# Optimization experiments

Measured on AMD Instinct MI355X. Metric: run time of the kernel, lower is better.

## Reference

```python
import jax, jax.numpy as jnp
import numpy as np

B, N, C = 2, 2048, 1024
H = 16
D = C // H  # head_dim = 64
HID = 4 * C
EPS = 1e-5


def _layernorm(x, g, b):
    mu = jnp.mean(x, axis=-1, keepdims=True)
    var = jnp.var(x, axis=-1, keepdims=True)
    return (x - mu) * jax.lax.rsqrt(var + EPS) * g + b


def _rope(x):
    # x: (B, H, N, D); interleaved-pair rotation, sin/cos computed in fp32
    half = D // 2
    inv_freq = 1.0 / (10000.0 ** (jnp.arange(half, dtype=jnp.float32) / half))
    pos = jnp.arange(N, dtype=jnp.float32)
    freqs = pos[:, None] * inv_freq[None, :]            # (N, half)
    sin = jnp.sin(freqs).astype(x.dtype)
    cos = jnp.cos(freqs).astype(x.dtype)
    xr = x.reshape(*x.shape[:-1], half, 2)
    x1, x2 = xr[..., 0], xr[..., 1]
    r1 = x1 * cos - x2 * sin
    r2 = x1 * sin + x2 * cos
    return jnp.stack((r1, r2), axis=-1).reshape(x.shape)


def setup_inputs() -> dict:
    key = jax.random.key(0)
    ks = jax.random.split(key, 8)
    s = lambda d: 1.0 / np.sqrt(d)
    return {
        "x": jax.random.normal(ks[0], (B, N, C), jnp.float32),
        "ln1_g": jnp.ones((C,), jnp.float32),
        "ln1_b": jnp.zeros((C,), jnp.float32),
        "W_qkv": jax.random.normal(ks[1], (C, 3 * C), jnp.float32) * s(C),
        "b_qkv": jnp.zeros((3 * C,), jnp.float32),
        "W_proj": jax.random.normal(ks[2], (C, C), jnp.float32) * s(C),
        "b_proj": jnp.zeros((C,), jnp.float32),
        "ln2_g": jnp.ones((C,), jnp.float32),
        "ln2_b": jnp.zeros((C,), jnp.float32),
        "W_fc1": jax.random.normal(ks[3], (C, HID), jnp.float32) * s(C),
        "b_fc1": jnp.zeros((HID,), jnp.float32),
        "W_fc2": jax.random.normal(ks[4], (HID, C), jnp.float32) * s(HID),
        "b_fc2": jnp.zeros((C,), jnp.float32),
    }


def reference(x, ln1_g, ln1_b, W_qkv, b_qkv, W_proj, b_proj,
              ln2_g, ln2_b, W_fc1, b_fc1, W_fc2, b_fc2):
    # --- attention branch ---
    h = _layernorm(x, ln1_g, ln1_b)
    qkv = h @ W_qkv + b_qkv                              # (B, N, 3C)
    qkv = qkv.reshape(B, N, 3, H, D).transpose(2, 0, 3, 1, 4)
    q, k, v = qkv[0], qkv[1], qkv[2]                     # each (B, H, N, D)
    q = _rope(q)
    k = _rope(k)
    scale = D ** -0.5
    attn = jnp.einsum('bhnd,bhmd->bhnm', q, k) * scale
    attn = jax.nn.softmax(attn, axis=-1)
    o = jnp.einsum('bhnm,bhmd->bhnd', attn, v)           # (B, H, N, D)
    o = o.transpose(0, 2, 1, 3).reshape(B, N, C)
    x = x + (o @ W_proj + b_proj)
    # --- MLP branch ---
    h = _layernorm(x, ln2_g, ln2_b)
    h = jax.nn.gelu(h @ W_fc1 + b_fc1, approximate=False)
    x = x + (h @ W_fc2 + b_fc2)
    return x
```

## Files before the change

kernel.cpp:

```cpp
#include <hip/hip_runtime.h>
#include <cstdint>
#include <cstddef>

typedef unsigned short u16;
typedef unsigned int   u32;
typedef __attribute__((ext_vector_type(8))) short v8s;
typedef __attribute__((ext_vector_type(4))) float v4f;

#define B_   2
#define N_   2048
#define C_   1024
#define H_   16
#define D_   64
#define HID_ 4096
#define M_   4096

static __device__ __forceinline__ float b2f(u32 u) {
    union { u32 i; float f; } x; x.i = u << 16; return x.f;
}
static __device__ __forceinline__ u16 f2b(float f) {
    union { float f; u32 i; } x; x.f = f;
    u32 r = (x.i + 0x7fffu + ((x.i >> 16) & 1u)) >> 16;
    return (u16)r;
}
static __device__ __forceinline__ u32 scale2(u32 raw, float s) {
    float lo = b2f(raw & 0xffffu) * s, hi = b2f(raw >> 16) * s;
    return (u32)f2b(lo) | ((u32)f2b(hi) << 16);
}

static __device__ __forceinline__ void gload_lds16(const u16* g, u16* l) {
    __builtin_amdgcn_global_load_lds(
        (const __attribute__((address_space(1))) void*)g,
        (__attribute__((address_space(3))) void*)l,
        16, 0, 0);
}

static __device__ __forceinline__ int2 xcd_swz(int gx, int gy) {
    const int nwg = gx * gy;
    int id = blockIdx.y * gx + blockIdx.x;
    id = (id & 7) * (nwg >> 3) + (id >> 3);
    return make_int2(id % gx, id / gx);
}

__global__ __launch_bounds__(256) void transpose_all(const float* __restrict__ Wqkv,
                                                     const float* __restrict__ Wproj,
                                                     const float* __restrict__ Wfc1,
                                                     const float* __restrict__ Wfc2,
                                                     u16* __restrict__ Oqkv,
                                                     u16* __restrict__ Oproj,
                                                     u16* __restrict__ Ofc1,
                                                     u16* __restrict__ Ofc2) {
    __shared__ float tile[32][33];
    int id = blockIdx.x;
    const float* in; u16* out; int K, N, nx;
    if (id < 3072)      { in = Wqkv;  out = Oqkv;  K = 1024; N = 3072; nx = 96;  }
    else if (id < 4096) { in = Wproj; out = Oproj; K = 1024; N = 1024; nx = 32;  id -= 3072; }
    else if (id < 8192) { in = Wfc1;  out = Ofc1;  K = 1024; N = 4096; nx = 128; id -= 4096; }
    else                { in = Wfc2;  out = Ofc2;  K = 4096; N = 1024; nx = 32;  id -= 8192; }
    const int n0 = (id % nx) * 32, k0 = (id / nx) * 32;
    const int c = threadIdx.x & 31, r8 = threadIdx.x >> 5;
#pragma unroll
    for (int i = 0; i < 4; ++i)
        tile[r8 + i * 8][c] = in[(size_t)(k0 + r8 + i * 8) * N + n0 + c];
    __syncthreads();
#pragma unroll
    for (int i = 0; i < 4; ++i)
        out[(size_t)(n0 + r8 + i * 8) * K + k0 + c] = f2b(tile[c][r8 + i * 8]);
}

__global__ __launch_bounds__(256) void ln_kernel(const float* __restrict__ in,
                                                 const float* __restrict__ g,
                                                 const float* __restrict__ b,
                                                 u16* __restrict__ out) {
    __shared__ float ps[4], psq[4];
    __shared__ float stats[2];
    const int row = blockIdx.x;
    const int t = threadIdx.x;
    float4 v = ((const float4*)in)[(size_t)row * 256 + t];
    float s  = v.x + v.y + v.z + v.w;
    float sq = v.x * v.x + v.y * v.y + v.z * v.z + v.w * v.w;
#pragma unroll
    for (int off = 32; off > 0; off >>= 1) { s += __shfl_down(s, off); sq += __shfl_down(sq, off); }
    if ((t & 63) == 0) { ps[t >> 6] = s; psq[t >> 6] = sq; }
    __syncthreads();
    if (t == 0) {
        float S = ps[0] + ps[1] + ps[2] + ps[3];
        float Q = psq[0] + psq[1] + psq[2] + psq[3];
        float mu  = S * (1.f / 1024.f);
        float var = Q * (1.f / 1024.f) - mu * mu;
        stats[0] = mu; stats[1] = rsqrtf(var + 1e-5f);
    }
    __syncthreads();
    const float mu = stats[0], istd = stats[1];
    float4 gg = ((const float4*)g)[t];
    float4 bb = ((const float4*)b)[t];
    ushort4 o;
    o.x = f2b((v.x - mu) * istd * gg.x + bb.x);
    o.y = f2b((v.y - mu) * istd * gg.y + bb.y);
    o.z = f2b((v.z - mu) * istd * gg.z + bb.z);
    o.w = f2b((v.w - mu) * istd * gg.w + bb.w);
    *(ushort4*)&out[(size_t)row * 1024 + t * 4] = o;
}

__global__ __launch_bounds__(256) void rope_table(float2* __restrict__ tab) {
    const int i = blockIdx.x * 256 + threadIdx.x;
    const int d = i & 31, n = i >> 5;
    float inv = powf(10000.f, -(float)d * (1.f / 32.f));
    float fr = (float)n * inv;
    tab[i] = make_float2(cosf(fr), sinf(fr));
}

template <int EPI, int BM>
__global__ __launch_bounds__(256) void gemm_bt(const u16* __restrict__ A,
                                               const u16* __restrict__ Bt,
                                               const float* __restrict__ bias,
                                               void* __restrict__ outp,
                                               const float* __restrict__ resid,
                                               const float2* __restrict__ tab,
                                               int Ndim, int Kdim) {
    constexpr int NACC = (BM == 128) ? 4 : 2;
    constexpr int AISS = BM / 64;
    __shared__ u16 As[3][BM * 32];
    __shared__ u16 Bs[3][128 * 32];
    const int t = threadIdx.x;
    const int lane = t & 63;
    const int w = t >> 6;
    const int wr = (BM == 128) ? (w >> 1) : 0;
    const int wc = (BM == 128) ? (w & 1) : w;
    const int2 lb = xcd_swz(gridDim.x, gridDim.y);
    const int m0 = lb.y * BM, n0 = lb.x * 128;
    const int hi = lane >> 4, lo = lane & 15;

    auto STAGE = [&](int buf, int kt) {
#pragma unroll
        for (int j = 0; j < AISS; ++j) {
            const int c = (w * AISS + j) * 64 + lane;
            gload_lds16(&A[(size_t)(m0 + (c >> 2)) * Kdim + kt + (c & 3) * 8],
                        &As[buf][(w * AISS + j) * 512]);
        }
#pragma unroll
        for (int j = 0; j < 2; ++j) {
            const int c = (w * 2 + j) * 64 + lane;
            gload_lds16(&Bt[(size_t)(n0 + (c >> 2)) * Kdim + kt + (c & 3) * 8],
                        &Bs[buf][(w * 2 + j) * 512]);
        }
    };

    const v4f vzero = {0.f, 0.f, 0.f, 0.f};
    v4f acc[4][NACC];
#pragma unroll
    for (int i = 0; i < 4; ++i)
#pragma unroll
        for (int j = 0; j < NACC; ++j) acc[i][j] = vzero;

    const int nt = Kdim / 32;
    STAGE(0, 0);
    STAGE(1, 32);
    for (int kt = 0; kt < nt; ++kt) {
        if constexpr (BM == 128) asm volatile("s_waitcnt vmcnt(4)" ::: "memory");
        else                     asm volatile("s_waitcnt vmcnt(3)" ::: "memory");
        __builtin_amdgcn_s_barrier();
        if (kt + 2 < nt) STAGE((kt + 2) % 3, (kt + 2) * 32);
        const int cur = kt % 3;
        v8s av[4], bv[NACC];
#pragma unroll
        for (int mi = 0; mi < 4; ++mi)
            av[mi] = *(const v8s*)&As[cur][(wr * 64 + mi * 16 + lo) * 32 + hi * 8];
#pragma unroll
        for (int ni = 0; ni < NACC; ++ni)
            bv[ni] = *(const v8s*)&Bs[cur][(wc * (NACC * 16) + ni * 16 + lo) * 32 + hi * 8];
#pragma unroll
        for (int mi = 0; mi < 4; ++mi)
#pragma unroll
            for (int ni = 0; ni < NACC; ++ni)
                acc[mi][ni] = __builtin_amdgcn_mfma_f32_16x16x32_bf16(av[mi], bv[ni], acc[mi][ni], 0, 0, 0);
    }

#pragma unroll
    for (int mi = 0; mi < 4; ++mi)
#pragma unroll
        for (int ni = 0; ni < NACC; ++ni) {
            const int col = n0 + wc * (NACC * 16) + ni * 16 + lo;
            const float bsv = bias[col];
#pragma unroll
            for (int r = 0; r < 4; ++r) {
                const int row = m0 + wr * 64 + mi * 16 + hi * 4 + r;
                float vacc = acc[mi][ni][r] + bsv;
                if (EPI == 0) {
                    const float partner = __shfl_xor(vacc, 1);
                    const int s = col >> 10;
                    if (s < 2) {
                        const int d = col & 63;
                        const int n = row & 2047;
                        float2 cs = tab[n * 32 + (d >> 1)];
                        vacc = vacc * cs.x + ((d & 1) ? partner * cs.y : -partner * cs.y);
                    }
                    const int rem = col & 1023, hh = rem >> 6, dd = rem & 63;
                    const int bb = row >> 11, nn = row & 2047;
                    ((u16*)outp)[((((size_t)s * B_ + bb) * H_ + hh) * N_ + nn) * D_ + dd] = f2b(vacc);
                } else if (EPI == 1) {
                    ((float*)outp)[(size_t)row * Ndim + col] = vacc + resid[(size_t)row * Ndim + col];
                } else {
                    const float gv = 0.5f * vacc * (1.f + erff(vacc * 0.70710678118f));
                    ((u16*)outp)[(size_t)row * Ndim + col] = f2b(gv);
                }
            }
        }
}

__global__ __launch_bounds__(512, 2) void gemm256_gelu(const u16* __restrict__ A,
                                                       const u16* __restrict__ Bt,
                                                       const float* __restrict__ bias,
                                                       u16* __restrict__ outp,
                                                       int Ndim, int Kdim) {
    __shared__ u16 As[2 * 2 * 256 * 32];
    __shared__ u16 Bs[2 * 2 * 256 * 32];
    const int t = threadIdx.x;
    const int lane = t & 63;
    const int w = t >> 6;
    const int wr = w >> 2, wc = w & 3;
    const int hi = lane >> 4, lo = lane & 15;
    const int2 lb = xcd_swz(gridDim.x, gridDim.y);
    const int m0 = lb.y * 256, n0 = lb.x * 256;
    const int koff = (hi * 8) ^ ((lo & 2) << 3);

    auto STAGEH = [&](u16* lds, const u16* src, int rb, int b, int ks, int kt) {
#pragma unroll
        for (int j = 0; j < 2; ++j) {
            const int c = j * 512 + t;
            const int row = c >> 2;
            const int e0 = (c & 3) * 8;
            gload_lds16(&src[(size_t)(rb + row) * Kdim + kt * 64 + ks * 32 + (e0 ^ ((row & 2) << 3))],
                        &lds[(b * 2 + ks) * 8192 + c * 8]);
        }
    };
    auto RD = [&](const u16* lds, int b, int ks, int row) -> v8s {
        return *(const v8s*)&lds[(b * 2 + ks) * 8192 + row * 32 + koff];
    };

    const v4f vzero = {0.f, 0.f, 0.f, 0.f};
    v4f acc[8][4];
#pragma unroll
    for (int i = 0; i < 8; ++i)
#pragma unroll
        for (int j = 0; j < 4; ++j) acc[i][j] = vzero;

    const int nt = Kdim / 64;
    STAGEH(As, A, m0, 0, 0, 0);
    STAGEH(Bs, Bt, n0, 0, 0, 0);
    STAGEH(As, A, m0, 0, 1, 0);
    STAGEH(Bs, Bt, n0, 0, 1, 0);

    for (int I = 0; I < nt; ++I) {
        const int b = I & 1, nb = b ^ 1;
        const bool pf = (I + 1 < nt);
        v8s av[4], bv[4];
        asm volatile("s_waitcnt vmcnt(4)" ::: "memory");
        __builtin_amdgcn_s_barrier();
#pragma unroll
        for (int n = 0; n < 4; ++n) bv[n] = RD(Bs, b, 0, wc * 64 + n * 16 + lo);
#pragma unroll
        for (int m = 0; m < 4; ++m) av[m] = RD(As, b, 0, wr * 128 + m * 16 + lo);
        if (pf) STAGEH(As, A, m0, nb, 0, I + 1);
        __builtin_amdgcn_s_setprio(1);
#pragma unroll
        for (int m = 0; m < 4; ++m)
#pragma unroll
            for (int n = 0; n < 4; ++n)
                acc[m][n] = __builtin_amdgcn_mfma_f32_16x16x32_bf16(av[m], bv[n], acc[m][n], 0, 0, 0);
        __builtin_amdgcn_s_setprio(0);
        __builtin_amdgcn_s_barrier();
#pragma unroll
        for (int m = 0; m < 4; ++m) av[m] = RD(As, b, 0, wr * 128 + 64 + m * 16 + lo);
        if (pf) STAGEH(Bs, Bt, n0, nb, 0, I + 1);
        __builtin_amdgcn_s_setprio(1);
#pragma unroll
        for (int m = 0; m < 4; ++m)
#pragma unroll
            for (int n = 0; n < 4; ++n)
                acc[4 + m][n] = __builtin_amdgcn_mfma_f32_16x16x32_bf16(av[m], bv[n], acc[4 + m][n], 0, 0, 0);
        __builtin_amdgcn_s_setprio(0);
        asm volatile("s_waitcnt vmcnt(4)" ::: "memory");
        __builtin_amdgcn_s_barrier();
#pragma unroll
        for (int n = 0; n < 4; ++n) bv[n] = RD(Bs, b, 1, wc * 64 + n * 16 + lo);
#pragma unroll
        for (int m = 0; m < 4; ++m) av[m] = RD(As, b, 1, wr * 128 + m * 16 + lo);
        if (pf) STAGEH(As, A, m0, nb, 1, I + 1);
        __builtin_amdgcn_s_setprio(1);
#pragma unroll
        for (int m = 0; m < 4; ++m)
#pragma unroll
            for (int n = 0; n < 4; ++n)
                acc[m][n] = __builtin_amdgcn_mfma_f32_16x16x32_bf16(av[m], bv[n], acc[m][n], 0, 0, 0);
        __builtin_amdgcn_s_setprio(0);
        __builtin_amdgcn_s_barrier();
#pragma unroll
        for (int m = 0; m < 4; ++m) av[m] = RD(As, b, 1, wr * 128 + 64 + m * 16 + lo);
        if (pf) STAGEH(Bs, Bt, n0, nb, 1, I + 1);
        __builtin_amdgcn_s_setprio(1);
#pragma unroll
        for (int m = 0; m < 4; ++m)
#pragma unroll
            for (int n = 0; n < 4; ++n)
                acc[4 + m][n] = __builtin_amdgcn_mfma_f32_16x16x32_bf16(av[m], bv[n], acc[4 + m][n], 0, 0, 0);
        __builtin_amdgcn_s_setprio(0);
    }

#pragma unroll
    for (int mi = 0; mi < 8; ++mi)
#pragma unroll
        for (int ni = 0; ni < 4; ++ni) {
            const int col = n0 + wc * 64 + ni * 16 + lo;
            const float bsv = bias[col];
#pragma unroll
            for (int r = 0; r < 4; ++r) {
                const int row = m0 + wr * 128 + mi * 16 + hi * 4 + r;
                float vacc = acc[mi][ni][r] + bsv;
                const float gv = 0.5f * vacc * (1.f + erff(vacc * 0.70710678118f));
                outp[(size_t)row * Ndim + col] = f2b(gv);
            }
        }
}

#define SCL_LOG2E 0.1803368801111244f
#define FIXEDM    12.0f

__global__ __launch_bounds__(256) void attn_mfma(const u16* __restrict__ q,
                                                 const u16* __restrict__ k,
                                                 const u16* __restrict__ v,
                                                 u16* __restrict__ out) {
    __shared__ u16 Ks[2][64 * 64];
    __shared__ u16 Vt[2][64 * 64];
    __shared__ u16 Ps[4][32 * 64];

    const int t    = threadIdx.x;
    const int w    = t >> 6;
    const int lane = t & 63;
    const int hi   = lane >> 4;
    const int lo   = lane & 15;
    const int2 lb  = xcd_swz(gridDim.x, gridDim.y);
    const int bh   = lb.y;
    const int r0g  = lb.x * 128 + w * 32;

    const u16* qb = q + (size_t)bh * N_ * D_;
    const u16* kb = k + (size_t)bh * N_ * D_;
    const u16* vb = v + (size_t)bh * N_ * D_;

    v8s qa[2][2];
#pragma unroll
    for (int mi = 0; mi < 2; ++mi)
#pragma unroll
        for (int ks = 0; ks < 2; ++ks) {
            uint4 rq = *(const uint4*)&qb[(size_t)(r0g + mi * 16 + lo) * 64 + ks * 32 + hi * 8];
            u32 qs[4];
            qs[0] = scale2(rq.x, SCL_LOG2E); qs[1] = scale2(rq.y, SCL_LOG2E);
            qs[2] = scale2(rq.z, SCL_LOG2E); qs[3] = scale2(rq.w, SCL_LOG2E);
            qa[mi][ks] = *(v8s*)qs;
        }

    u32 ones4[4] = {0x3F803F80u, 0x3F803F80u, 0x3F803F80u, 0x3F803F80u};
    const v8s ones = *(v8s*)ones4;

    const v4f vzero = {0.f, 0.f, 0.f, 0.f};
    const v4f cinit = {-FIXEDM, -FIXEDM, -FIXEDM, -FIXEDM};
    v4f o_acc[2][4];
    v4f l_acc[2];
#pragma unroll
    for (int mi = 0; mi < 2; ++mi) {
        l_acc[mi] = vzero;
#pragma unroll
        for (int ni = 0; ni < 4; ++ni) o_acc[mi][ni] = vzero;
    }

    const int vp = t & 31, vg = t >> 5;
    const int vd0 = vg * 8, vkey = vp * 2;

    uint4 kreg[2], vr0, vr1;
    auto LOADT = [&](int kt) {
#pragma unroll
        for (int i = 0; i < 2; ++i) {
            const int chunk = i * 256 + t;
            kreg[i] = *(const uint4*)&kb[(size_t)(kt * 64 + (chunk >> 3)) * 64 + (chunk & 7) * 8];
        }
        vr0 = *(const uint4*)&vb[(size_t)(kt * 64 + vkey) * 64 + vd0];
        vr1 = *(const uint4*)&vb[(size_t)(kt * 64 + vkey + 1) * 64 + vd0];
    };
    auto WRITET = [&](int buf) {
#pragma unroll
        for (int i = 0; i < 2; ++i) {
            const int chunk = i * 256 + t;
            const int key = chunk >> 3, d0 = (chunk & 7) * 8;
            *(uint4*)&Ks[buf][key * 64 + (d0 ^ ((key & 7) << 3))] = kreg[i];
        }
        const u32* a0 = (const u32*)&vr0;
        const u32* a1 = (const u32*)&vr1;
#pragma unroll
        for (int j = 0; j < 8; ++j) {
            u32 lo16 = (j & 1) ? (a0[j >> 1] >> 16) : (a0[j >> 1] & 0xffffu);
            u32 hi16 = (j & 1) ? (a1[j >> 1] >> 16) : (a1[j >> 1] & 0xffffu);
            u32 val = lo16 | (hi16 << 16);
            *(u32*)&Vt[buf][(vd0 + j) * 64 + (vkey ^ (j << 3))] = val;
        }
    };

    LOADT(0);
    WRITET(0);
    __syncthreads();

    for (int kt = 0; kt < N_ / 64; ++kt) {
        const int cb = kt & 1;
        const bool pf = (kt + 1 < N_ / 64);
        if (pf) LOADT(kt + 1);

        v4f s[2][4];
#pragma unroll
        for (int mi = 0; mi < 2; ++mi)
#pragma unroll
            for (int ni = 0; ni < 4; ++ni) s[mi][ni] = cinit;
        __builtin_amdgcn_s_setprio(1);
#pragma unroll
        for (int ks = 0; ks < 2; ++ks)
#pragma unroll
            for (int ni = 0; ni < 4; ++ni) {
                const int key = lo + 16 * ni;
                v8s bv = *(const v8s*)&Ks[cb][key * 64 + ((ks * 32 + hi * 8) ^ ((key & 7) << 3))];
                s[0][ni] = __builtin_amdgcn_mfma_f32_16x16x32_bf16(qa[0][ks], bv, s[0][ni], 0, 0, 0);
                s[1][ni] = __builtin_amdgcn_mfma_f32_16x16x32_bf16(qa[1][ks], bv, s[1][ni], 0, 0, 0);
            }
        __builtin_amdgcn_s_setprio(0);

#pragma unroll
        for (int mi = 0; mi < 2; ++mi)
#pragma unroll
            for (int ni = 0; ni < 4; ++ni)
#pragma unroll
                for (int r = 0; r < 4; ++r)
                    s[mi][ni][r] = exp2f(s[mi][ni][r]);

#pragma unroll
        for (int mi = 0; mi < 2; ++mi)
#pragma unroll
            for (int f = 0; f < 4; ++f)
#pragma unroll
                for (int rp = 0; rp < 2; ++rp) {
                    u32 pk;
                    asm("v_cvt_pk_bf16_f32 %0, %1, %2"
                        : "=v"(pk) : "v"(s[mi][f][2 * rp]), "v"(s[mi][f][2 * rp + 1]));
                    const int row0 = mi * 16 + hi * 4 + 2 * rp;
                    const int row1 = row0 + 1;
                    Ps[w][row0 * 64 + ((lo + 16 * f) ^ ((row0 & 7) << 3))] = (u16)pk;
                    Ps[w][row1 * 64 + ((lo + 16 * f) ^ ((row1 & 7) << 3))] = (u16)(pk >> 16);
                }
        v8s pa[2][2];
#pragma unroll
        for (int mi = 0; mi < 2; ++mi)
#pragma unroll
            for (int ks = 0; ks < 2; ++ks) {
                const int row = mi * 16 + lo;
                pa[mi][ks] = *(const v8s*)&Ps[w][row * 64 + ((ks * 32 + hi * 8) ^ ((lo & 7) << 3))];
            }

        __builtin_amdgcn_s_setprio(1);
#pragma unroll
        for (int ks = 0; ks < 2; ++ks) {
#pragma unroll
            for (int ni = 0; ni < 4; ++ni) {
                const int dim = lo + 16 * ni;
                v8s vv = *(const v8s*)&Vt[cb][dim * 64 + ((ks * 32 + hi * 8) ^ ((dim & 7) << 3))];
                o_acc[0][ni] = __builtin_amdgcn_mfma_f32_16x16x32_bf16(pa[0][ks], vv, o_acc[0][ni], 0, 0, 0);
                o_acc[1][ni] = __builtin_amdgcn_mfma_f32_16x16x32_bf16(pa[1][ks], vv, o_acc[1][ni], 0, 0, 0);
            }
            l_acc[0] = __builtin_amdgcn_mfma_f32_16x16x32_bf16(pa[0][ks], ones, l_acc[0], 0, 0, 0);
            l_acc[1] = __builtin_amdgcn_mfma_f32_16x16x32_bf16(pa[1][ks], ones, l_acc[1], 0, 0, 0);
        }
        __builtin_amdgcn_s_setprio(0);

        if (pf) WRITET(cb ^ 1);
        __syncthreads();
    }

    const int bb = bh >> 4, hh = bh & 15;
#pragma unroll
    for (int mi = 0; mi < 2; ++mi)
#pragma unroll
        for (int r = 0; r < 4; ++r) {
            const float inv = 1.f / l_acc[mi][r];
            const int n = r0g + mi * 16 + hi * 4 + r;
#pragma unroll
            for (int ni = 0; ni < 4; ++ni) {
                out[((size_t)bb * N_ + n) * C_ + hh * D_ + lo + 16 * ni] = f2b(o_acc[mi][ni][r] * inv);
            }
        }
}

extern "C" void kernel_launch(void* const* d_in, const int* in_sizes, int n_in,
                              void* d_out, int out_size, void* d_ws, size_t ws_size,
                              hipStream_t stream) {
    (void)in_sizes; (void)n_in; (void)out_size; (void)ws_size;
    const float* x     = (const float*)d_in[0];
    const float* ln1g  = (const float*)d_in[1];
    const float* ln1b  = (const float*)d_in[2];
    const float* Wqkv  = (const float*)d_in[3];
    const float* bqkv  = (const float*)d_in[4];
    const float* Wproj = (const float*)d_in[5];
    const float* bproj = (const float*)d_in[6];
    const float* ln2g  = (const float*)d_in[7];
    const float* ln2b  = (const float*)d_in[8];
    const float* Wfc1  = (const float*)d_in[9];
    const float* bfc1  = (const float*)d_in[10];
    const float* Wfc2  = (const float*)d_in[11];
    const float* bfc2  = (const float*)d_in[12];
    float* out = (float*)d_out;

    char* base = (char*)d_ws;
    const size_t MB = 1024 * 1024;
    u16* Wtqkv  = (u16*)(base);
    u16* Wtproj = (u16*)(base + 6 * MB);
    u16* Wtfc1  = (u16*)(base + 8 * MB);
    u16* Wtfc2  = (u16*)(base + 16 * MB);
    u16* qkv    = (u16*)(base + 24 * MB);
    u16* a1     = (u16*)(base + 24 * MB);
    u16* h1     = (u16*)(base + 56 * MB);
    u16* oatt   = (u16*)(base + 56 * MB);
    u16* h2     = (u16*)(base + 56 * MB);
    float* x1   = (float*)(base + 64 * MB);
    float2* tab = (float2*)(base + 80 * MB);

    transpose_all<<<12288, 256, 0, stream>>>(Wqkv, Wproj, Wfc1, Wfc2,
                                             Wtqkv, Wtproj, Wtfc1, Wtfc2);
    rope_table<<<N_ * (D_ / 2) / 256, 256, 0, stream>>>(tab);
    ln_kernel<<<M_, 256, 0, stream>>>(x, ln1g, ln1b, h1);
    gemm_bt<0, 128><<<dim3(3 * C_ / 128, M_ / 128), 256, 0, stream>>>(h1, Wtqkv, bqkv, qkv, nullptr, tab, 3 * C_, C_);
    attn_mfma<<<dim3(N_ / 128, B_ * H_), 256, 0, stream>>>(
        qkv, qkv + (size_t)B_ * H_ * N_ * D_, qkv + (size_t)2 * B_ * H_ * N_ * D_, oatt);
    gemm_bt<1, 64><<<dim3(C_ / 128, M_ / 64), 256, 0, stream>>>(oatt, Wtproj, bproj, x1, x, nullptr, C_, C_);
    ln_kernel<<<M_, 256, 0, stream>>>(x1, ln2g, ln2b, h2);
    gemm256_gelu<<<dim3(HID_ / 256, M_ / 256), 512, 0, stream>>>(h2, Wtfc1, bfc1, a1, HID_, C_);
    gemm_bt<1, 64><<<dim3(C_ / 128, M_ / 64), 256, 0, stream>>>(a1, Wtfc2, bfc2, out, x1, nullptr, C_, HID_);
}
```

Before: 285.8 us.

## Add BK=64 swizzled GEMM for residual projections and async K staging in attention

Adds a new gemm_bk64 kernel with a 64-wide K tile, XOR-swizzled LDS layout and a three-buffer async global-to-LDS pipeline. It replaces gemm_bt for the attention projection and the FC2 GEMM. The attention kernel now stages K tiles straight into LDS with async loads instead of going through registers, while V keeps its register transpose path. The waitcnt counts on the last iterations are also fixed to drain all outstanding loads, which trades a slightly longer final wait for correctness of the tail loads.

```diff
diff --git a/kernel.cpp b/kernel.cpp
--- a/kernel.cpp
+++ b/kernel.cpp
@@ -157,8 +157,9 @@
     STAGE(0, 0);
     STAGE(1, 32);
     for (int kt = 0; kt < nt; ++kt) {
-        if constexpr (BM == 128) asm volatile("s_waitcnt vmcnt(4)" ::: "memory");
-        else                     asm volatile("s_waitcnt vmcnt(3)" ::: "memory");
+        if (kt + 1 == nt) asm volatile("s_waitcnt vmcnt(0)" ::: "memory");
+        else if constexpr (BM == 128) asm volatile("s_waitcnt vmcnt(4)" ::: "memory");
+        else                          asm volatile("s_waitcnt vmcnt(3)" ::: "memory");
         __builtin_amdgcn_s_barrier();
         if (kt + 2 < nt) STAGE((kt + 2) % 3, (kt + 2) * 32);
         const int cur = kt % 3;
@@ -208,6 +209,87 @@
         }
 }
 
+__global__ __launch_bounds__(256) void gemm_bk64(const u16* __restrict__ A,
+                                                 const u16* __restrict__ Bt,
+                                                 const float* __restrict__ bias,
+                                                 float* __restrict__ outp,
+                                                 const float* __restrict__ resid,
+                                                 int Ndim, int Kdim) {
+    __shared__ u16 As[3][64 * 64];
+    __shared__ u16 Bs[3][128 * 64];
+    const int t = threadIdx.x;
+    const int lane = t & 63;
+    const int w = t >> 6;
+    const int2 lb = xcd_swz(gridDim.x, gridDim.y);
+    const int m0 = lb.y * 64, n0 = lb.x * 128;
+    const int hi = lane >> 4, lo = lane & 15;
+
+    auto STAGE = [&](int buf, int kb) {
+#pragma unroll
+        for (int j = 0; j < 2; ++j) {
+            const int c = (w * 2 + j) * 64 + lane;
+            const int row = c >> 3, ch = c & 7;
+            gload_lds16(&A[(size_t)(m0 + row) * Kdim + kb + ((ch ^ (row & 7)) * 8)],
+                        &As[buf][(w * 2 + j) * 512]);
+        }
+#pragma unroll
+        for (int j = 0; j < 4; ++j) {
+            const int c = (w * 4 + j) * 64 + lane;
+            const int row = c >> 3, ch = c & 7;
+            gload_lds16(&Bt[(size_t)(n0 + row) * Kdim + kb + ((ch ^ (row & 7)) * 8)],
+                        &Bs[buf][(w * 4 + j) * 512]);
+        }
+    };
+
+    const v4f vzero = {0.f, 0.f, 0.f, 0.f};
+    v4f acc[4][2];
+#pragma unroll
+    for (int i = 0; i < 4; ++i) { acc[i][0] = vzero; acc[i][1] = vzero; }
+
+    const int nt = Kdim / 64;
+    STAGE(0, 0);
+    STAGE(1, 64);
+    for (int kt = 0; kt < nt; ++kt) {
+        if (kt + 1 == nt) asm volatile("s_waitcnt vmcnt(0)" ::: "memory");
+        else              asm volatile("s_waitcnt vmcnt(6)" ::: "memory");
+        __builtin_amdgcn_s_barrier();
+        if (kt + 2 < nt) STAGE((kt + 2) % 3, (kt + 2) * 64);
+        const int cur = kt % 3;
+#pragma unroll
+        for (int ks = 0; ks < 2; ++ks) {
+            v8s av[4], bv[2];
+#pragma unroll
+            for (int m = 0; m < 4; ++m) {
+                const int row = m * 16 + lo;
+                av[m] = *(const v8s*)&As[cur][row * 64 + (((ks * 4 + hi) ^ (row & 7)) * 8)];
+            }
+#pragma unroll
+            for (int n = 0; n < 2; ++n) {
+                const int row = w * 32 + n * 16 + lo;
+                bv[n] = *(const v8s*)&Bs[cur][row * 64 + (((ks * 4 + hi) ^ (row & 7)) * 8)];
+            }
+#pragma unroll
+            for (int m = 0; m < 4; ++m)
+#pragma unroll
+                for (int n = 0; n < 2; ++n)
+                    acc[m][n] = __builtin_amdgcn_mfma_f32_16x16x32_bf16(av[m], bv[n], acc[m][n], 0, 0, 0);
+        }
+    }
+
+#pragma unroll
+    for (int m = 0; m < 4; ++m)
+#pragma unroll
+        for (int n = 0; n < 2; ++n) {
+            const int col = n0 + w * 32 + n * 16 + lo;
+            const float bsv = bias[col];
+#pragma unroll
+            for (int r = 0; r < 4; ++r) {
+                const int row = m0 + m * 16 + hi * 4 + r;
+                outp[(size_t)row * Ndim + col] = acc[m][n][r] + bsv + resid[(size_t)row * Ndim + col];
+            }
+        }
+}
+
 __global__ __launch_bounds__(512, 2) void gemm256_gelu(const u16* __restrict__ A,
                                                        const u16* __restrict__ Bt,
                                                        const float* __restrict__ bias,
@@ -255,7 +337,8 @@
         const int b = I & 1, nb = b ^ 1;
         const bool pf = (I + 1 < nt);
         v8s av[4], bv[4];
-        asm volatile("s_waitcnt vmcnt(4)" ::: "memory");
+        if (pf) asm volatile("s_waitcnt vmcnt(4)" ::: "memory");
+        else    asm volatile("s_waitcnt vmcnt(2)" ::: "memory");
         __builtin_amdgcn_s_barrier();
 #pragma unroll
         for (int n = 0; n < 4; ++n) bv[n] = RD(Bs, b, 0, wc * 64 + n * 16 + lo);
@@ -280,7 +363,8 @@
             for (int n = 0; n < 4; ++n)
                 acc[4 + m][n] = __builtin_amdgcn_mfma_f32_16x16x32_bf16(av[m], bv[n], acc[4 + m][n], 0, 0, 0);
         __builtin_amdgcn_s_setprio(0);
-        asm volatile("s_waitcnt vmcnt(4)" ::: "memory");
+        if (pf) asm volatile("s_waitcnt vmcnt(4)" ::: "memory");
+        else    asm volatile("s_waitcnt vmcnt(0)" ::: "memory");
         __builtin_amdgcn_s_barrier();
 #pragma unroll
         for (int n = 0; n < 4; ++n) bv[n] = RD(Bs, b, 1, wc * 64 + n * 16 + lo);
@@ -376,23 +460,21 @@
     const int vp = t & 31, vg = t >> 5;
     const int vd0 = vg * 8, vkey = vp * 2;
 
-    uint4 kreg[2], vr0, vr1;
-    auto LOADT = [&](int kt) {
-#pragma unroll
-        for (int i = 0; i < 2; ++i) {
-            const int chunk = i * 256 + t;
-            kreg[i] = *(const uint4*)&kb[(size_t)(kt * 64 + (chunk >> 3)) * 64 + (chunk & 7) * 8];
-        }
+    auto KSTAGE = [&](int buf, int kt) {
+#pragma unroll
+        for (int j = 0; j < 2; ++j) {
+            const int c = (w * 2 + j) * 64 + lane;
+            const int key = c >> 3, ch = c & 7;
+            gload_lds16(&kb[(size_t)(kt * 64 + key) * 64 + ((ch ^ (key & 7)) * 8)],
+                        &Ks[buf][(w * 2 + j) * 512]);
+        }
+    };
+    uint4 vr0, vr1;
+    auto LOADV = [&](int kt) {
         vr0 = *(const uint4*)&vb[(size_t)(kt * 64 + vkey) * 64 + vd0];
         vr1 = *(const uint4*)&vb[(size_t)(kt * 64 + vkey + 1) * 64 + vd0];
     };
-    auto WRITET = [&](int buf) {
-#pragma unroll
-        for (int i = 0; i < 2; ++i) {
-            const int chunk = i * 256 + t;
-            const int key = chunk >> 3, d0 = (chunk & 7) * 8;
-            *(uint4*)&Ks[buf][key * 64 + (d0 ^ ((key & 7) << 3))] = kreg[i];
-        }
+    auto WRITEV = [&](int buf) {
         const u32* a0 = (const u32*)&vr0;
         const u32* a1 = (const u32*)&vr1;
 #pragma unroll
@@ -404,14 +486,15 @@
         }
     };
 
-    LOADT(0);
-    WRITET(0);
+    KSTAGE(0, 0);
+    LOADV(0);
+    WRITEV(0);
     __syncthreads();
 
     for (int kt = 0; kt < N_ / 64; ++kt) {
         const int cb = kt & 1;
         const bool pf = (kt + 1 < N_ / 64);
-        if (pf) LOADT(kt + 1);
+        if (pf) { KSTAGE(cb ^ 1, kt + 1); LOADV(kt + 1); }
 
         v4f s[2][4];
 #pragma unroll
@@ -476,7 +559,7 @@
         }
         __builtin_amdgcn_s_setprio(0);
 
-        if (pf) WRITET(cb ^ 1);
+        if (pf) WRITEV(cb ^ 1);
         __syncthreads();
     }
 
@@ -534,8 +617,8 @@
     gemm_bt<0, 128><<<dim3(3 * C_ / 128, M_ / 128), 256, 0, stream>>>(h1, Wtqkv, bqkv, qkv, nullptr, tab, 3 * C_, C_);
     attn_mfma<<<dim3(N_ / 128, B_ * H_), 256, 0, stream>>>(
         qkv, qkv + (size_t)B_ * H_ * N_ * D_, qkv + (size_t)2 * B_ * H_ * N_ * D_, oatt);
-    gemm_bt<1, 64><<<dim3(C_ / 128, M_ / 64), 256, 0, stream>>>(oatt, Wtproj, bproj, x1, x, nullptr, C_, C_);
+    gemm_bk64<<<dim3(C_ / 128, M_ / 64), 256, 0, stream>>>(oatt, Wtproj, bproj, x1, x, C_, C_);
     ln_kernel<<<M_, 256, 0, stream>>>(x1, ln2g, ln2b, h2);
     gemm256_gelu<<<dim3(HID_ / 256, M_ / 256), 512, 0, stream>>>(h2, Wtfc1, bfc1, a1, HID_, C_);
-    gemm_bt<1, 64><<<dim3(C_ / 128, M_ / 64), 256, 0, stream>>>(a1, Wtfc2, bfc2, out, x1, nullptr, C_, HID_);
-}
+    gemm_bk64<<<dim3(C_ / 128, M_ / 64), 256, 0, stream>>>(a1, Wtfc2, bfc2, out, x1, C_, HID_);
+}
```

Result: faster. 276.1 us, median of 2 (-3.4%).
